# Performance work log

Hardware: AMD Instinct MI355X
Metric: run time of the kernel (lower is better)

Reference implementation:

```python
import jax, jax.numpy as jnp
import numpy as np
from jax import lax

KS = 3           # kernel size
PAD = 1          # padding
BN_EPS = 1e-5


def _conv(x, w, b):
    # plain stride-1, pad-1 NCHW conv
    y = lax.conv_general_dilated(x, w, window_strides=(1, 1),
                                 padding=[(PAD, PAD), (PAD, PAD)],
                                 dimension_numbers=("NCHW", "OIHW", "NCHW"))
    return y + b[None, :, None, None]


def _deform_conv(x, offset, mask, w_reg):
    # x: [B,C,H,W]; offset: [B,2K,H,W] (dy,dx interleaved); mask: [B,K,H,W]
    B, C, H, W = x.shape
    K = KS * KS
    dy = offset[:, 0::2]  # [B,K,H,W]
    dx = offset[:, 1::2]
    base_ky = jnp.repeat(jnp.arange(KS), KS).astype(x.dtype)   # [K]
    base_kx = jnp.tile(jnp.arange(KS), KS).astype(x.dtype)
    gy = (jnp.arange(H) - PAD).astype(x.dtype)
    gx = (jnp.arange(W) - PAD).astype(x.dtype)
    py = base_ky[None, :, None, None] + gy[None, None, :, None] + dy  # [B,K,H,W]
    px = base_kx[None, :, None, None] + gx[None, None, None, :] + dx

    y0 = jnp.floor(py); x0 = jnp.floor(px)
    wy = py - y0;       wx = px - x0
    x_flat = x.reshape(B, C, H * W)

    def gather(yi, xi):
        valid = (yi >= 0) & (yi < H) & (xi >= 0) & (xi < W)
        yc = jnp.clip(yi, 0, H - 1).astype(jnp.int32)
        xc = jnp.clip(xi, 0, W - 1).astype(jnp.int32)
        idx = (yc * W + xc).reshape(B, 1, K * H * W)
        v = jnp.take_along_axis(x_flat, jnp.broadcast_to(idx, (B, C, K * H * W)), axis=2)
        v = v.reshape(B, C, K, H, W)
        return v * valid[:, None].astype(x.dtype)

    sampled = ((1 - wy) * (1 - wx))[:, None] * gather(y0, x0) \
            + ((1 - wy) * wx)[:, None]       * gather(y0, x0 + 1) \
            + (wy * (1 - wx))[:, None]       * gather(y0 + 1, x0) \
            + (wy * wx)[:, None]             * gather(y0 + 1, x0 + 1)
    sampled = sampled * mask[:, None]  # modulation, [B,C,K,H,W]
    Cout = w_reg.shape[0]
    return jnp.einsum("bckhw,ock->bohw", sampled, w_reg.reshape(Cout, C, K))


def setup_inputs() -> dict:
    key = jax.random.key(0)
    ks = jax.random.split(key, 9)
    B, Cin, Cout, H, W = 4, 256, 256, 64, 64
    K = KS * KS
    inp = {
        "x": jax.random.normal(ks[0], (B, Cin, H, W), jnp.float32),
        # offset / modulator conv params (zero-init in source; small random for meaningful test)
        "w_off": jax.random.normal(ks[1], (2 * K, Cin, KS, KS), jnp.float32) * 0.01,
        "b_off": jax.random.normal(ks[2], (2 * K,), jnp.float32) * 0.01,
        "w_mod": jax.random.normal(ks[3], (K, Cin, KS, KS), jnp.float32) * 0.01,
        "b_mod": jax.random.normal(ks[4], (K,), jnp.float32) * 0.01,
        # regular conv weight (bias=False)
        "w_reg": jax.random.normal(ks[5], (Cout, Cin, KS, KS), jnp.float32) * (1.0 / np.sqrt(Cin * K)),
        # BatchNorm (inference mode: running stats)
        "gamma": jnp.ones((Cout,), jnp.float32),
        "beta": jnp.zeros((Cout,), jnp.float32),
        "run_mean": jax.random.normal(ks[6], (Cout,), jnp.float32) * 0.1,
        "run_var": jax.random.uniform(ks[7], (Cout,), jnp.float32, 0.5, 1.5),
    }
    return inp


def reference(x, w_off, b_off, w_mod, b_mod, w_reg, gamma, beta, run_mean, run_var):
    offset = _conv(x, w_off, b_off)                       # [B,2K,H,W]
    mask = 2.0 * jax.nn.sigmoid(_conv(x, w_mod, b_mod))   # [B,K,H,W]
    y = _deform_conv(x, offset, mask, w_reg)              # [B,Cout,H,W]
    inv = gamma / jnp.sqrt(run_var + BN_EPS)
    y = y * inv[None, :, None, None] + (beta - run_mean * inv)[None, :, None, None]
    return jax.nn.relu(y)
```

## Files before the change

kernel.cpp:

```cpp
#include <hip/hip_runtime.h>
#include <hip/hip_bf16.h>

typedef unsigned short u16;
typedef unsigned int   u32;
typedef short   bf16x8 __attribute__((ext_vector_type(8)));
typedef float   f32x4  __attribute__((ext_vector_type(4)));

__device__ __forceinline__ float bf2f(u16 u) {
    u32 t = ((u32)u) << 16;
    return __builtin_bit_cast(float, t);
}
__device__ __forceinline__ u32 f2bf(float f) {
    u32 u = __builtin_bit_cast(u32, f);
    return (u + 0x7FFFu + ((u >> 16) & 1u)) >> 16;
}
__device__ __forceinline__ void load_lds16(const u16* g, u16* l) {
    __builtin_amdgcn_global_load_lds(
        (const __attribute__((address_space(1))) u32*)(const void*)g,
        (__attribute__((address_space(3))) u32*)(void*)l, 16, 0, 0);
}
__device__ __forceinline__ uint4 gload4(const u16* sbase, u32 voff) {
    uint4 r;
    asm volatile("global_load_dwordx4 %0, %1, %2"
                 : "=v"(r) : "v"(voff), "s"(sbase) : "memory");
    return r;
}
__device__ __forceinline__ f32x4 gload4f(const float* sbase, u32 voff) {
    f32x4 r;
    asm volatile("global_load_dwordx4 %0, %1, %2"
                 : "=v"(r) : "v"(voff), "s"(sbase) : "memory");
    return r;
}
#define WAITVM(N) do { asm volatile("s_waitcnt vmcnt(" #N ")" ::: "memory"); \
                       __builtin_amdgcn_sched_barrier(0); } while (0)


__global__ void kprep(const float* __restrict__ woff, const float* __restrict__ wmod,
                      u16* __restrict__ ah, u16* __restrict__ al) {
    int i = blockIdx.x * 256 + threadIdx.x;
    if (i >= 32 * 2304) return;
    int oc = i / 2304, r = i - oc * 2304;
    int t = r >> 8, c = r & 255;
    float v = 0.f;
    if (oc < 18)      v = woff[oc * 2304 + c * 9 + t];
    else if (oc < 27) v = wmod[(oc - 18) * 2304 + c * 9 + t];
    u32 hb = f2bf(v);
    u32 lb = f2bf(v - bf2f((u16)hb));
    ah[i] = (u16)hb;
    al[i] = (u16)lb;
}

__global__ void kwreg(const float* __restrict__ wreg, u16* __restrict__ wregb) {
    int i = blockIdx.x * 256 + threadIdx.x;
    int o = i / 2304, r = i - o * 2304;
    int t = r >> 8, c = r & 255;
    wregb[i] = (u16)f2bf(wreg[o * 2304 + c * 9 + t]);
}

__global__ __launch_bounds__(256) void ktrans(const float* __restrict__ x,
                                              float* __restrict__ xt) {
    __shared__ float T[64][65];
    int t = threadIdx.x;
    int pl = t & 63, cr = t >> 6;
    int p0 = blockIdx.x * 64;
    int c0 = blockIdx.y * 64;
    int b  = blockIdx.z;
    const float* xb  = x  + ((long)b << 20);
    float*       xtb = xt + ((long)b << 20);
#pragma unroll
    for (int i = 0; i < 16; i++) {
        int c = cr + i * 4;
        T[c][pl] = xb[((long)(c0 + c) << 12) + p0 + pl];
    }
    __syncthreads();
#pragma unroll
    for (int i = 0; i < 16; i++) {
        int p = cr + i * 4;
        xtb[(long)(p0 + p) * 256 + c0 + pl] = T[pl][p];
    }
}

__global__ __launch_bounds__(512, 4) void koffg(const float* __restrict__ xt,
                                                const u16* __restrict__ ah_g,
                                                const u16* __restrict__ al_g,
                                                const float* __restrict__ boff,
                                                const float* __restrict__ bmod,
                                                float* __restrict__ offf) {
    __shared__ u16 Ah[4][32 * 72], Al[4][32 * 72];
    __shared__ u16 Bh[4][32 * 72], Bl[4][32 * 72];
    int tid = threadIdx.x;
    int ltid = tid & 255, kg = tid >> 8;
    int bid = blockIdx.x;
    int xcd = bid & 7, j = bid >> 3;
    int img = xcd >> 1;
    int row = ((xcd & 1) << 5) + (j >> 1);
    int n0 = ((img << 6) + row) * 64 + (j & 1) * 32;
    int b = n0 >> 12, h0 = (n0 & 4095) >> 6, w0 = n0 & 63;
    int lane = tid & 63, wv = tid >> 6;
    int mt = wv & 1, nt = (wv >> 1) & 1;
    int col = lane & 15, quad = lane >> 4;

    int aoc = ltid >> 3, ak0 = (ltid & 7) * 8;
    int chq = lane & 15, pxs = lane >> 4;
    int px0 = (wv & 3) * 4 + pxs, px1 = px0 + 16;

    int ktb = kg * 18;

    const float* xtb = xt + ((long)b << 20);
    u32 avoff0 = (u32)(aoc * 2304 + ak0) * 2;

    f32x4 acc = (f32x4){0.f, 0.f, 0.f, 0.f};

    uint4 pah, pal;
    f32x4 xa, xc;
    bool  vma, vmb;

    auto issue = [&](int kt) {
        int t = kt >> 2, c0 = (kt & 3) << 6, r0 = kt * 64;
        int dy = t / 3 - 1, dx = t % 3 - 1;
        pah = gload4(ah_g, avoff0 + (u32)r0 * 2);
        pal = gload4(al_g, avoff0 + (u32)r0 * 2);
        int hp = h0 + dy;
        bool vh = (unsigned)hp < 64u;
        int hc = min(max(hp, 0), 63);
        u32 cb = (u32)(c0 + chq * 4) << 2;
        int wpa = w0 + px0 + dx;
        vma = vh && ((unsigned)wpa < 64u);
        int wca = min(max(wpa, 0), 63);
        xa = gload4f(xtb, ((u32)(hc * 64 + wca) << 10) + cb);
        int wpb = w0 + px1 + dx;
        vmb = vh && ((unsigned)wpb < 64u);
        int wcb = min(max(wpb, 0), 63);
        xc = gload4f(xtb, ((u32)(hc * 64 + wcb) << 10) + cb);
    };
    auto stores = [&](int buf) {
        int sb = kg * 2 + buf;
        *(uint4*)&Ah[sb][aoc * 72 + ak0] = pah;
        *(uint4*)&Al[sb][aoc * 72 + ak0] = pal;
        u32 wh[2], wl[2];
#pragma unroll
        for (int i = 0; i < 4; i++) {
            float v = vma ? xa[i] : 0.f;
            u32 hb = f2bf(v);
            u32 lb = f2bf(v - bf2f((u16)hb));
            if (i & 1) { wh[i >> 1] |= hb << 16; wl[i >> 1] |= lb << 16; }
            else       { wh[i >> 1]  = hb;       wl[i >> 1]  = lb; }
        }
        *(uint2*)&Bh[sb][px0 * 72 + chq * 4] = make_uint2(wh[0], wh[1]);
        *(uint2*)&Bl[sb][px0 * 72 + chq * 4] = make_uint2(wl[0], wl[1]);
#pragma unroll
        for (int i = 0; i < 4; i++) {
            float v = vmb ? xc[i] : 0.f;
            u32 hb = f2bf(v);
            u32 lb = f2bf(v - bf2f((u16)hb));
            if (i & 1) { wh[i >> 1] |= hb << 16; wl[i >> 1] |= lb << 16; }
            else       { wh[i >> 1]  = hb;       wl[i >> 1]  = lb; }
        }
        *(uint2*)&Bh[sb][px1 * 72 + chq * 4] = make_uint2(wh[0], wh[1]);
        *(uint2*)&Bl[sb][px1 * 72 + chq * 4] = make_uint2(wl[0], wl[1]);
    };

    issue(ktb + 0);
    WAITVM(0);
    stores(0);
    issue(ktb + 1);
    asm volatile("s_waitcnt lgkmcnt(0)" ::: "memory");
    __builtin_amdgcn_s_barrier();
    __builtin_amdgcn_sched_barrier(0);

    for (int kt = 0; kt < 18; kt++) {
        int cur = kt & 1, nxt = kt + 1;
        int sb = kg * 2 + cur;
#pragma unroll
        for (int ks = 0; ks < 2; ks++) {
            int ko = ks * 32 + quad * 8;
            bf16x8 fah = *(const bf16x8*)&Ah[sb][(mt * 16 + col) * 72 + ko];
            bf16x8 fal = *(const bf16x8*)&Al[sb][(mt * 16 + col) * 72 + ko];
            bf16x8 fbh = *(const bf16x8*)&Bh[sb][(nt * 16 + col) * 72 + ko];
            bf16x8 fbl = *(const bf16x8*)&Bl[sb][(nt * 16 + col) * 72 + ko];
            acc = __builtin_amdgcn_mfma_f32_16x16x32_bf16(fah, fbh, acc, 0, 0, 0);
            acc = __builtin_amdgcn_mfma_f32_16x16x32_bf16(fah, fbl, acc, 0, 0, 0);
            acc = __builtin_amdgcn_mfma_f32_16x16x32_bf16(fal, fbh, acc, 0, 0, 0);
        }
        if (nxt < 18) {
            WAITVM(0);
            stores(nxt & 1);
            if (nxt + 1 < 18) issue(ktb + nxt + 1);
        }
        asm volatile("s_waitcnt lgkmcnt(0)" ::: "memory");
        __builtin_amdgcn_s_barrier();
        __builtin_amdgcn_sched_barrier(0);
    }

    float* scratch = (float*)&Ah[0][0];
    if (kg) *(f32x4*)&scratch[ltid * 4] = acc;
    __syncthreads();
    if (kg == 0) {
        f32x4 o = *(const f32x4*)&scratch[ltid * 4];
        acc += o;
        int n = n0 + nt * 16 + col;
#pragma unroll
        for (int r = 0; r < 4; r++) {
            int oc = mt * 16 + quad * 4 + r;
            float s = acc[r];
            if (oc < 18) {
                int ch = 3 * (oc >> 1) + (oc & 1);
                offf[(ch << 14) + n] = s + boff[oc];
            } else if (oc < 27) {
                float tt = s + bmod[oc - 18];
                int ch = 3 * (oc - 18) + 2;
                offf[(ch << 14) + n] = 2.f / (1.f + __expf(-tt));
            }
        }
    }
}

__global__ __launch_bounds__(512, 4) void kfused(const float* __restrict__ xt,
                                                 const float* __restrict__ offf,
                                                 const u16* __restrict__ wregb,
                                                 const float* __restrict__ gamma,
                                                 const float* __restrict__ beta,
                                                 const float* __restrict__ rmean,
                                                 const float* __restrict__ rvar,
                                                 float* __restrict__ out) {
    __shared__ u16 Wl[2][256 * 64];
    __shared__ u16 Sl[2][8 * 32 * 8];
    int tid = threadIdx.x;
    int lane = tid & 63, wv = tid >> 6;
    int chq = lane & 15;
    int plo = wv * 4 + (lane >> 4);
    int bid = blockIdx.x;
    int xcd = bid & 7, jj = bid >> 3;
    int bb  = xcd >> 1;
    int h   = ((xcd & 1) << 5) + (jj >> 1);
    int nbase = ((bb << 6) + h) * 64 + (jj & 1) * 32;
    int wo = wv * 32;
    int col = lane & 15, quad = lane >> 4;

    const float* xb = xt + ((long)bb << 20);

    f32x4 acc[2][2];
#pragma unroll
    for (int i = 0; i < 2; i++)
#pragma unroll
        for (int j = 0; j < 2; j++) acc[i][j] = (f32x4){0.f, 0.f, 0.f, 0.f};

    u32   pb[4];
    float sw[4];
    f32x4 g[4];

    auto tapcomp = [&](int t) {
        int n = nbase + plo;
        int w = n & 63;
        int gy = t / 3, tx = t - 3 * gy;
        float dy = offf[((3 * t + 0) << 14) + n];
        float dx = offf[((3 * t + 1) << 14) + n];
        float m  = offf[((3 * t + 2) << 14) + n];
        float py = (float)(h - 1 + gy) + dy;
        float px = (float)(w - 1 + tx) + dx;
        float y0f = floorf(py), x0f = floorf(px);
        float wy = py - y0f, wx = px - x0f;
        int iy0 = (int)y0f, ix0 = (int)x0f;
        int iy1 = iy0 + 1, ix1 = ix0 + 1;
        bool vy0 = (unsigned)iy0 < 64u, vy1 = (unsigned)iy1 < 64u;
        bool vx0 = (unsigned)ix0 < 64u, vx1 = (unsigned)ix1 < 64u;
        int cy0 = min(max(iy0, 0), 63), cy1 = min(max(iy1, 0), 63);
        int cx0 = min(max(ix0, 0), 63), cx1 = min(max(ix1, 0), 63);
        pb[0] = (u32)(cy0 * 64 + cx0) << 10; pb[1] = (u32)(cy0 * 64 + cx1) << 10;
        pb[2] = (u32)(cy1 * 64 + cx0) << 10; pb[3] = (u32)(cy1 * 64 + cx1) << 10;
        float a = 1.f - wy, bw = 1.f - wx;
        sw[0] = (vy0 && vx0) ? a  * bw * m : 0.f;
        sw[1] = (vy0 && vx1) ? a  * wx * m : 0.f;
        sw[2] = (vy1 && vx0) ? wy * bw * m : 0.f;
        sw[3] = (vy1 && vx1) ? wy * wx * m : 0.f;
    };
    auto gissue = [&](int kt) {
        u32 co = ((u32)(kt & 3) << 8) + (u32)chq * 16;
#pragma unroll
        for (int nb = 0; nb < 4; nb++) g[nb] = gload4f(xb, pb[nb] + co);
    };
    auto dmaA = [&](int kt, int buf) {
#pragma unroll
        for (int i = 0; i < 4; i++) {
            int cidx = tid + i * 512;
            int o = cidx >> 3, qp = cidx & 7;
            int ql = qp ^ (o & 7);
            load_lds16(wregb + (long)o * 2304 + kt * 64 + ql * 8,
                       &Wl[buf][cidx * 8]);
        }
    };
    auto bwrite = [&](int buf) {
        f32x4 v = sw[0] * g[0] + sw[1] * g[1] + sw[2] * g[2] + sw[3] * g[3];
        u32 w0 = f2bf(v[0]) | (f2bf(v[1]) << 16);
        u32 w1 = f2bf(v[2]) | (f2bf(v[3]) << 16);
        *(uint2*)&Sl[buf][((chq >> 1) * 32 + plo) * 8 + (chq & 1) * 4] =
            make_uint2(w0, w1);
    };

    tapcomp(0);
    gissue(0);
    dmaA(0, 0);
    WAITVM(0);
    bwrite(0);
    __syncthreads();

    for (int kt = 0; kt < 36; kt++) {
        int cur = kt & 1, nxt = kt + 1;
        if (nxt < 36) {
            if ((nxt & 3) == 0) tapcomp(nxt >> 2);
            gissue(nxt);
            dmaA(nxt, nxt & 1);
        }
#pragma unroll
        for (int ks = 0; ks < 2; ks++) {
            bf16x8 af[2], bfr[2];
#pragma unroll
            for (int i = 0; i < 2; i++) {
                int r = wo + i * 16 + col;
                int ph = (ks * 4 + quad) ^ (r & 7);
                af[i] = *(const bf16x8*)&Wl[cur][r * 64 + ph * 8];
            }
#pragma unroll
            for (int j = 0; j < 2; j++)
                bfr[j] = *(const bf16x8*)&Sl[cur][((ks * 4 + quad) * 32 +
                                                   (j * 16 + col)) * 8];
#pragma unroll
            for (int i = 0; i < 2; i++)
#pragma unroll
                for (int j = 0; j < 2; j++)
                    acc[i][j] = __builtin_amdgcn_mfma_f32_16x16x32_bf16(
                        af[i], bfr[j], acc[i][j], 0, 0, 0);
        }
        if (nxt < 36) {
            WAITVM(4);
            bwrite(nxt & 1);
        }
        __syncthreads();
    }

#pragma unroll
    for (int i = 0; i < 2; i++) {
        int ob = wo + i * 16 + quad * 4;
        float inv[4], add[4];
#pragma unroll
        for (int r = 0; r < 4; r++) {
            int o = ob + r;
            float iv = gamma[o] * rsqrtf(rvar[o] + 1e-5f);
            inv[r] = iv; add[r] = beta[o] - rmean[o] * iv;
        }
#pragma unroll
        for (int j = 0; j < 2; j++) {
            int n_g = nbase + j * 16 + col;
            int bq = n_g >> 12, hw = n_g & 4095;
            float* op = out + ((long)bq << 20) + hw;
#pragma unroll
            for (int r = 0; r < 4; r++) {
                float v = acc[i][j][r] * inv[r] + add[r];
                v = fmaxf(v, 0.f);
                op[(long)(ob + r) << 12] = v;
            }
        }
    }
}

extern "C" void kernel_launch(void* const* d_in, const int* in_sizes, int n_in,
                              void* d_out, int out_size, void* d_ws, size_t ws_size,
                              hipStream_t stream) {
    const float* x     = (const float*)d_in[0];
    const float* woff  = (const float*)d_in[1];
    const float* boff  = (const float*)d_in[2];
    const float* wmod  = (const float*)d_in[3];
    const float* bmod  = (const float*)d_in[4];
    const float* wreg  = (const float*)d_in[5];
    const float* gamma = (const float*)d_in[6];
    const float* beta  = (const float*)d_in[7];
    const float* rmean = (const float*)d_in[8];
    const float* rvar  = (const float*)d_in[9];
    float* out = (float*)d_out;

    char* ws = (char*)d_ws;
    u16*   wph   = (u16*)(ws);
    u16*   wpl   = (u16*)(ws + 0x40000u);
    float* offf  = (float*)(ws + 0x80000u);
    u16*   wregb = (u16*)(ws + 0x240000u);
    float* xt    = (float*)(ws + 0x400000u);

    kprep<<<288,  256, 0, stream>>>(woff, wmod, wph, wpl);
    kwreg<<<2304, 256, 0, stream>>>(wreg, wregb);
    ktrans<<<dim3(64, 4, 4), 256, 0, stream>>>(x, xt);
    koffg<<<512,  512, 0, stream>>>(xt, wph, wpl, boff, bmod, offf);
    kfused<<<512, 512, 0, stream>>>(xt, offf, wregb, gamma, beta,
                                    rmean, rvar, out);
}
```

Before: 176.9 us.

## Fuse offset/modulator conv into deformable conv kernel via shared memory

Merges the offset/mask generation GEMM into the main deformable-conv kernel. Each block first computes the offsets and mask for its own 32 pixels into LDS, then reuses a shared scratch buffer for the weight and sample tiles. This drops one kernel launch and the global round trip of the offset tensor. In exchange the shared-memory footprint is larger and the two phases run serially within each block, which may lower occupancy.

```diff
diff --git a/kernel.cpp b/kernel.cpp
--- a/kernel.cpp
+++ b/kernel.cpp
@@ -80,164 +80,155 @@
     }
 }
 
-__global__ __launch_bounds__(512, 4) void koffg(const float* __restrict__ xt,
-                                                const u16* __restrict__ ah_g,
-                                                const u16* __restrict__ al_g,
-                                                const float* __restrict__ boff,
-                                                const float* __restrict__ bmod,
-                                                float* __restrict__ offf) {
-    __shared__ u16 Ah[4][32 * 72], Al[4][32 * 72];
-    __shared__ u16 Bh[4][32 * 72], Bl[4][32 * 72];
-    int tid = threadIdx.x;
-    int ltid = tid & 255, kg = tid >> 8;
-    int bid = blockIdx.x;
-    int xcd = bid & 7, j = bid >> 3;
-    int img = xcd >> 1;
-    int row = ((xcd & 1) << 5) + (j >> 1);
-    int n0 = ((img << 6) + row) * 64 + (j & 1) * 32;
-    int b = n0 >> 12, h0 = (n0 & 4095) >> 6, w0 = n0 & 63;
-    int lane = tid & 63, wv = tid >> 6;
-    int mt = wv & 1, nt = (wv >> 1) & 1;
-    int col = lane & 15, quad = lane >> 4;
-
-    int aoc = ltid >> 3, ak0 = (ltid & 7) * 8;
-    int chq = lane & 15, pxs = lane >> 4;
-    int px0 = (wv & 3) * 4 + pxs, px1 = px0 + 16;
-
-    int ktb = kg * 18;
-
-    const float* xtb = xt + ((long)b << 20);
-    u32 avoff0 = (u32)(aoc * 2304 + ak0) * 2;
-
-    f32x4 acc = (f32x4){0.f, 0.f, 0.f, 0.f};
-
-    uint4 pah, pal;
-    f32x4 xa, xc;
-    bool  vma, vmb;
-
-    auto issue = [&](int kt) {
-        int t = kt >> 2, c0 = (kt & 3) << 6, r0 = kt * 64;
-        int dy = t / 3 - 1, dx = t % 3 - 1;
-        pah = gload4(ah_g, avoff0 + (u32)r0 * 2);
-        pal = gload4(al_g, avoff0 + (u32)r0 * 2);
-        int hp = h0 + dy;
-        bool vh = (unsigned)hp < 64u;
-        int hc = min(max(hp, 0), 63);
-        u32 cb = (u32)(c0 + chq * 4) << 2;
-        int wpa = w0 + px0 + dx;
-        vma = vh && ((unsigned)wpa < 64u);
-        int wca = min(max(wpa, 0), 63);
-        xa = gload4f(xtb, ((u32)(hc * 64 + wca) << 10) + cb);
-        int wpb = w0 + px1 + dx;
-        vmb = vh && ((unsigned)wpb < 64u);
-        int wcb = min(max(wpb, 0), 63);
-        xc = gload4f(xtb, ((u32)(hc * 64 + wcb) << 10) + cb);
-    };
-    auto stores = [&](int buf) {
-        int sb = kg * 2 + buf;
-        *(uint4*)&Ah[sb][aoc * 72 + ak0] = pah;
-        *(uint4*)&Al[sb][aoc * 72 + ak0] = pal;
-        u32 wh[2], wl[2];
-#pragma unroll
-        for (int i = 0; i < 4; i++) {
-            float v = vma ? xa[i] : 0.f;
-            u32 hb = f2bf(v);
-            u32 lb = f2bf(v - bf2f((u16)hb));
-            if (i & 1) { wh[i >> 1] |= hb << 16; wl[i >> 1] |= lb << 16; }
-            else       { wh[i >> 1]  = hb;       wl[i >> 1]  = lb; }
-        }
-        *(uint2*)&Bh[sb][px0 * 72 + chq * 4] = make_uint2(wh[0], wh[1]);
-        *(uint2*)&Bl[sb][px0 * 72 + chq * 4] = make_uint2(wl[0], wl[1]);
-#pragma unroll
-        for (int i = 0; i < 4; i++) {
-            float v = vmb ? xc[i] : 0.f;
-            u32 hb = f2bf(v);
-            u32 lb = f2bf(v - bf2f((u16)hb));
-            if (i & 1) { wh[i >> 1] |= hb << 16; wl[i >> 1] |= lb << 16; }
-            else       { wh[i >> 1]  = hb;       wl[i >> 1]  = lb; }
-        }
-        *(uint2*)&Bh[sb][px1 * 72 + chq * 4] = make_uint2(wh[0], wh[1]);
-        *(uint2*)&Bl[sb][px1 * 72 + chq * 4] = make_uint2(wl[0], wl[1]);
-    };
-
-    issue(ktb + 0);
-    WAITVM(0);
-    stores(0);
-    issue(ktb + 1);
-    asm volatile("s_waitcnt lgkmcnt(0)" ::: "memory");
-    __builtin_amdgcn_s_barrier();
-    __builtin_amdgcn_sched_barrier(0);
-
-    for (int kt = 0; kt < 18; kt++) {
-        int cur = kt & 1, nxt = kt + 1;
-        int sb = kg * 2 + cur;
-#pragma unroll
-        for (int ks = 0; ks < 2; ks++) {
-            int ko = ks * 32 + quad * 8;
-            bf16x8 fah = *(const bf16x8*)&Ah[sb][(mt * 16 + col) * 72 + ko];
-            bf16x8 fal = *(const bf16x8*)&Al[sb][(mt * 16 + col) * 72 + ko];
-            bf16x8 fbh = *(const bf16x8*)&Bh[sb][(nt * 16 + col) * 72 + ko];
-            bf16x8 fbl = *(const bf16x8*)&Bl[sb][(nt * 16 + col) * 72 + ko];
-            acc = __builtin_amdgcn_mfma_f32_16x16x32_bf16(fah, fbh, acc, 0, 0, 0);
-            acc = __builtin_amdgcn_mfma_f32_16x16x32_bf16(fah, fbl, acc, 0, 0, 0);
-            acc = __builtin_amdgcn_mfma_f32_16x16x32_bf16(fal, fbh, acc, 0, 0, 0);
-        }
-        if (nxt < 18) {
-            WAITVM(0);
-            stores(nxt & 1);
-            if (nxt + 1 < 18) issue(ktb + nxt + 1);
-        }
-        asm volatile("s_waitcnt lgkmcnt(0)" ::: "memory");
-        __builtin_amdgcn_s_barrier();
-        __builtin_amdgcn_sched_barrier(0);
-    }
-
-    float* scratch = (float*)&Ah[0][0];
-    if (kg) *(f32x4*)&scratch[ltid * 4] = acc;
-    __syncthreads();
-    if (kg == 0) {
-        f32x4 o = *(const f32x4*)&scratch[ltid * 4];
-        acc += o;
-        int n = n0 + nt * 16 + col;
-#pragma unroll
-        for (int r = 0; r < 4; r++) {
-            int oc = mt * 16 + quad * 4 + r;
-            float s = acc[r];
-            if (oc < 18) {
-                int ch = 3 * (oc >> 1) + (oc & 1);
-                offf[(ch << 14) + n] = s + boff[oc];
-            } else if (oc < 27) {
-                float tt = s + bmod[oc - 18];
-                int ch = 3 * (oc - 18) + 2;
-                offf[(ch << 14) + n] = 2.f / (1.f + __expf(-tt));
-            }
-        }
-    }
-}
-
 __global__ __launch_bounds__(512, 4) void kfused(const float* __restrict__ xt,
-                                                 const float* __restrict__ offf,
+                                                 const u16* __restrict__ ah_g,
+                                                 const u16* __restrict__ al_g,
+                                                 const float* __restrict__ boff,
+                                                 const float* __restrict__ bmod,
                                                  const u16* __restrict__ wregb,
                                                  const float* __restrict__ gamma,
                                                  const float* __restrict__ beta,
                                                  const float* __restrict__ rmean,
                                                  const float* __restrict__ rvar,
                                                  float* __restrict__ out) {
-    __shared__ u16 Wl[2][256 * 64];
-    __shared__ u16 Sl[2][8 * 32 * 8];
+    __shared__ char  smem[73728];
+    __shared__ float offl[27 * 32];
     int tid = threadIdx.x;
     int lane = tid & 63, wv = tid >> 6;
-    int chq = lane & 15;
-    int plo = wv * 4 + (lane >> 4);
+    int col = lane & 15, quad = lane >> 4;
     int bid = blockIdx.x;
     int xcd = bid & 7, jj = bid >> 3;
     int bb  = xcd >> 1;
     int h   = ((xcd & 1) << 5) + (jj >> 1);
     int nbase = ((bb << 6) + h) * 64 + (jj & 1) * 32;
+    int h0 = h, w0 = nbase & 63;
+    const float* xtb = xt + ((long)bb << 20);
+
+    {
+        u16* AH = (u16*)smem;
+        u16* AL = AH + 4 * 2304;
+        u16* BH = AL + 4 * 2304;
+        u16* BL = BH + 4 * 2304;
+
+        int ltid = tid & 255, kg = tid >> 8;
+        int mt = wv & 1, nt = (wv >> 1) & 1;
+        int aoc = ltid >> 3, ak0 = (ltid & 7) * 8;
+        int chq = lane & 15, pxs = lane >> 4;
+        int px0 = (wv & 3) * 4 + pxs, px1 = px0 + 16;
+        int ktb = kg * 18;
+        u32 avoff0 = (u32)(aoc * 2304 + ak0) * 2;
+
+        f32x4 acc = (f32x4){0.f, 0.f, 0.f, 0.f};
+        uint4 pah, pal;
+        f32x4 xa, xc;
+        bool  vma, vmb;
+
+        auto issue = [&](int kt) {
+            int t = kt >> 2, c0 = (kt & 3) << 6, r0 = kt * 64;
+            int dy = t / 3 - 1, dx = t % 3 - 1;
+            pah = gload4(ah_g, avoff0 + (u32)r0 * 2);
+            pal = gload4(al_g, avoff0 + (u32)r0 * 2);
+            int hp = h0 + dy;
+            bool vh = (unsigned)hp < 64u;
+            int hc = min(max(hp, 0), 63);
+            u32 cb = (u32)(c0 + chq * 4) << 2;
+            int wpa = w0 + px0 + dx;
+            vma = vh && ((unsigned)wpa < 64u);
+            int wca = min(max(wpa, 0), 63);
+            xa = gload4f(xtb, ((u32)(hc * 64 + wca) << 10) + cb);
+            int wpb = w0 + px1 + dx;
+            vmb = vh && ((unsigned)wpb < 64u);
+            int wcb = min(max(wpb, 0), 63);
+            xc = gload4f(xtb, ((u32)(hc * 64 + wcb) << 10) + cb);
+        };
+        auto stores = [&](int buf) {
+            int sb = kg * 2 + buf;
+            *(uint4*)&AH[sb * 2304 + aoc * 72 + ak0] = pah;
+            *(uint4*)&AL[sb * 2304 + aoc * 72 + ak0] = pal;
+            u32 wh[2], wl[2];
+#pragma unroll
+            for (int i = 0; i < 4; i++) {
+                float v = vma ? xa[i] : 0.f;
+                u32 hb = f2bf(v);
+                u32 lb = f2bf(v - bf2f((u16)hb));
+                if (i & 1) { wh[i >> 1] |= hb << 16; wl[i >> 1] |= lb << 16; }
+                else       { wh[i >> 1]  = hb;       wl[i >> 1]  = lb; }
+            }
+            *(uint2*)&BH[sb * 2304 + px0 * 72 + chq * 4] = make_uint2(wh[0], wh[1]);
+            *(uint2*)&BL[sb * 2304 + px0 * 72 + chq * 4] = make_uint2(wl[0], wl[1]);
+#pragma unroll
+            for (int i = 0; i < 4; i++) {
+                float v = vmb ? xc[i] : 0.f;
+                u32 hb = f2bf(v);
+                u32 lb = f2bf(v - bf2f((u16)hb));
+                if (i & 1) { wh[i >> 1] |= hb << 16; wl[i >> 1] |= lb << 16; }
+                else       { wh[i >> 1]  = hb;       wl[i >> 1]  = lb; }
+            }
+            *(uint2*)&BH[sb * 2304 + px1 * 72 + chq * 4] = make_uint2(wh[0], wh[1]);
+            *(uint2*)&BL[sb * 2304 + px1 * 72 + chq * 4] = make_uint2(wl[0], wl[1]);
+        };
+
+        issue(ktb + 0);
+        WAITVM(0);
+        stores(0);
+        issue(ktb + 1);
+        asm volatile("s_waitcnt lgkmcnt(0)" ::: "memory");
+        __builtin_amdgcn_s_barrier();
+        __builtin_amdgcn_sched_barrier(0);
+
+        for (int kt = 0; kt < 18; kt++) {
+            int cur = kt & 1, nxt = kt + 1;
+            int sb = kg * 2 + cur;
+#pragma unroll
+            for (int ks = 0; ks < 2; ks++) {
+                int ko = ks * 32 + quad * 8;
+                bf16x8 fah = *(const bf16x8*)&AH[sb * 2304 + (mt * 16 + col) * 72 + ko];
+                bf16x8 fal = *(const bf16x8*)&AL[sb * 2304 + (mt * 16 + col) * 72 + ko];
+                bf16x8 fbh = *(const bf16x8*)&BH[sb * 2304 + (nt * 16 + col) * 72 + ko];
+                bf16x8 fbl = *(const bf16x8*)&BL[sb * 2304 + (nt * 16 + col) * 72 + ko];
+                acc = __builtin_amdgcn_mfma_f32_16x16x32_bf16(fah, fbh, acc, 0, 0, 0);
+                acc = __builtin_amdgcn_mfma_f32_16x16x32_bf16(fah, fbl, acc, 0, 0, 0);
+                acc = __builtin_amdgcn_mfma_f32_16x16x32_bf16(fal, fbh, acc, 0, 0, 0);
+            }
+            if (nxt < 18) {
+                WAITVM(0);
+                stores(nxt & 1);
+                if (nxt + 1 < 18) issue(ktb + nxt + 1);
+            }
+            asm volatile("s_waitcnt lgkmcnt(0)" ::: "memory");
+            __builtin_amdgcn_s_barrier();
+            __builtin_amdgcn_sched_barrier(0);
+        }
+
+        float* scratch = (float*)AH;
+        if (kg) *(f32x4*)&scratch[ltid * 4] = acc;
+        __syncthreads();
+        if (kg == 0) {
+            f32x4 o = *(const f32x4*)&scratch[ltid * 4];
+            acc += o;
+            int lpx = nt * 16 + col;
+#pragma unroll
+            for (int r = 0; r < 4; r++) {
+                int oc = mt * 16 + quad * 4 + r;
+                float s = acc[r];
+                if (oc < 18) {
+                    int ch = 3 * (oc >> 1) + (oc & 1);
+                    offl[ch * 32 + lpx] = s + boff[oc];
+                } else if (oc < 27) {
+                    float tt = s + bmod[oc - 18];
+                    int ch = 3 * (oc - 18) + 2;
+                    offl[ch * 32 + lpx] = 2.f / (1.f + __expf(-tt));
+                }
+            }
+        }
+        __syncthreads();
+    }
+
+    u16* WL = (u16*)smem;
+    u16* SL = WL + 2 * 256 * 64;
+    int chq = lane & 15;
+    int plo = wv * 4 + (lane >> 4);
     int wo = wv * 32;
-    int col = lane & 15, quad = lane >> 4;
-
-    const float* xb = xt + ((long)bb << 20);
 
     f32x4 acc[2][2];
 #pragma unroll
@@ -250,12 +241,11 @@
     f32x4 g[4];
 
     auto tapcomp = [&](int t) {
-        int n = nbase + plo;
-        int w = n & 63;
+        int w = (nbase + plo) & 63;
         int gy = t / 3, tx = t - 3 * gy;
-        float dy = offf[((3 * t + 0) << 14) + n];
-        float dx = offf[((3 * t + 1) << 14) + n];
-        float m  = offf[((3 * t + 2) << 14) + n];
+        float dy = offl[(3 * t + 0) * 32 + plo];
+        float dx = offl[(3 * t + 1) * 32 + plo];
+        float m  = offl[(3 * t + 2) * 32 + plo];
         float py = (float)(h - 1 + gy) + dy;
         float px = (float)(w - 1 + tx) + dx;
         float y0f = floorf(py), x0f = floorf(px);
@@ -277,7 +267,7 @@
     auto gissue = [&](int kt) {
         u32 co = ((u32)(kt & 3) << 8) + (u32)chq * 16;
 #pragma unroll
-        for (int nb = 0; nb < 4; nb++) g[nb] = gload4f(xb, pb[nb] + co);
+        for (int nb = 0; nb < 4; nb++) g[nb] = gload4f(xtb, pb[nb] + co);
     };
     auto dmaA = [&](int kt, int buf) {
 #pragma unroll
@@ -286,14 +276,14 @@
             int o = cidx >> 3, qp = cidx & 7;
             int ql = qp ^ (o & 7);
             load_lds16(wregb + (long)o * 2304 + kt * 64 + ql * 8,
-                       &Wl[buf][cidx * 8]);
+                       &WL[buf * 16384 + cidx * 8]);
         }
     };
     auto bwrite = [&](int buf) {
         f32x4 v = sw[0] * g[0] + sw[1] * g[1] + sw[2] * g[2] + sw[3] * g[3];
         u32 w0 = f2bf(v[0]) | (f2bf(v[1]) << 16);
         u32 w1 = f2bf(v[2]) | (f2bf(v[3]) << 16);
-        *(uint2*)&Sl[buf][((chq >> 1) * 32 + plo) * 8 + (chq & 1) * 4] =
+        *(uint2*)&SL[buf * 2048 + ((chq >> 1) * 32 + plo) * 8 + (chq & 1) * 4] =
             make_uint2(w0, w1);
     };
 
@@ -318,12 +308,12 @@
             for (int i = 0; i < 2; i++) {
                 int r = wo + i * 16 + col;
                 int ph = (ks * 4 + quad) ^ (r & 7);
-                af[i] = *(const bf16x8*)&Wl[cur][r * 64 + ph * 8];
+                af[i] = *(const bf16x8*)&WL[cur * 16384 + r * 64 + ph * 8];
             }
 #pragma unroll
             for (int j = 0; j < 2; j++)
-                bfr[j] = *(const bf16x8*)&Sl[cur][((ks * 4 + quad) * 32 +
-                                                   (j * 16 + col)) * 8];
+                bfr[j] = *(const bf16x8*)&SL[cur * 2048 + ((ks * 4 + quad) * 32 +
+                                             (j * 16 + col)) * 8];
 #pragma unroll
             for (int i = 0; i < 2; i++)
 #pragma unroll
@@ -381,14 +371,12 @@
     char* ws = (char*)d_ws;
     u16*   wph   = (u16*)(ws);
     u16*   wpl   = (u16*)(ws + 0x40000u);
-    float* offf  = (float*)(ws + 0x80000u);
     u16*   wregb = (u16*)(ws + 0x240000u);
     float* xt    = (float*)(ws + 0x400000u);
 
     kprep<<<288,  256, 0, stream>>>(woff, wmod, wph, wpl);
     kwreg<<<2304, 256, 0, stream>>>(wreg, wregb);
     ktrans<<<dim3(64, 4, 4), 256, 0, stream>>>(x, xt);
-    koffg<<<512,  512, 0, stream>>>(xt, wph, wpl, boff, bmod, offf);
-    kfused<<<512, 512, 0, stream>>>(xt, offf, wregb, gamma, beta,
-                                    rmean, rvar, out);
-}
+    kfused<<<512, 512, 0, stream>>>(xt, wph, wpl, boff, bmod, wregb,
+                                    gamma, beta, rmean, rvar, out);
+}
```

After: 168.9 us. -4.5%, faster.
